# Optimization experiments

Measured on AMD Instinct MI355X. Metric: run time of the kernel, lower is better.

The kernel has to match this reference:

```python
import jax, jax.numpy as jnp
import numpy as np

B, CIN, HIN, WIN = 1, 26, 721, 1440
K, HOUT, KH, KW = 9, 360, 9, 9
COUT = 256
PSCALE = WIN // (WIN // 2)  # lon downsample stride = 2
WOUT = WIN // 2


def setup_inputs() -> dict:
    key = jax.random.key(0)
    k1, k2, k3 = jax.random.split(key, 3)
    x = jax.random.normal(k1, (B, CIN, HIN, WIN), dtype=jnp.float32)
    # precomputed basis*quadrature stencil psi[k, ho, dh, dw] (shift-invariant in lon,
    # stored only for wo=0, exactly as DISCO does). Normalized per (k, ho) ('mean' mode).
    psi = jax.random.normal(k2, (K, HOUT, KH, KW), dtype=jnp.float32)
    psi = psi / (jnp.mean(jnp.abs(psi), axis=(2, 3), keepdims=True) * (KH * KW) + 1e-6)
    weight = jax.random.normal(k3, (COUT, CIN, K), dtype=jnp.float32) * (1.0 / np.sqrt(CIN * K))
    # base input-lat row for each output lat (stencil top row), clipped to valid range
    hi_base = np.clip(np.round(np.arange(HOUT) * (HIN - 1) / HOUT).astype(np.int32) - KH // 2, 0, HIN - 1)
    return {"x": x, "psi": psi, "weight": weight, "hi_base": jnp.asarray(hi_base, dtype=jnp.int32)}


def _disco_conv(x, psi, weight, hi_base):
    x = x.astype(jnp.float32)  # fp32 autocast-off region, matches torch module
    acc = jnp.zeros((B, CIN, K, HOUT, WOUT), dtype=jnp.float32)
    for dh in range(KH):  # small structural loop over stencil rows
        rows = jnp.clip(hi_base + dh, 0, HIN - 1)  # [Hout]
        xr = x[:, :, rows, :]
        for dw in range(KW):  # small structural loop over stencil lon offsets
            shift = dw - KW // 2
            xs = jnp.roll(xr, -shift, axis=-1)[..., ::PSCALE]  # [B,C,Hout,Wout]
            acc = acc + psi[:, :, dh, dw][None, None, :, :, None] * xs[:, :, None, :, :]
    # contract learned weights over kernel basis and input channels
    out = jnp.einsum('bckhw,ock->bohw', acc, weight)  # [B,Cout,Hout,Wout]
    return out


def reference(x, psi, weight, hi_base):
    return _disco_conv(x, psi, weight, hi_base)
```

## Files before the change

kernel.cpp:

```cpp
#include <hip/hip_runtime.h>
#include <hip/hip_bf16.h>

#define CIN_   26
#define HIN_   721
#define WIN_   1440
#define K_     9
#define HOUT_  360
#define KH_    9
#define KW_    9
#define COUT_  256
#define WOUT_  720

#define WT     16
#define XSP    48
#define CCH    7
#define CK     (CIN_ * K_)
#define NKS2   9
#define ACCP2  296
#define NMT    (COUT_ / 16)
#define NXCD   8
#define HBAND  (HOUT_ / NXCD)

typedef short bf16x8 __attribute__((ext_vector_type(8)));
typedef float f32x4  __attribute__((ext_vector_type(4)));

__device__ unsigned short g_whi[NMT * NKS2 * 64 * 8];
__device__ unsigned short g_pfrag[HOUT_ * 3 * 64 * 8];

__device__ __forceinline__ unsigned short f2bf_rne(float f) {
    union { float f; unsigned u; } v; v.f = f;
    unsigned u = v.u;
    unsigned r = (u + 0x7FFFu + ((u >> 16) & 1u)) >> 16;
    return (unsigned short)r;
}
__device__ __forceinline__ unsigned pack_bf2(float a, float b) {
    const __hip_bfloat162 bv = __float22bfloat162_rn(make_float2(a, b));
    return *reinterpret_cast<const unsigned*>(&bv);
}

__global__ void prep_weight_kernel(const float* __restrict__ weight) {
    const int bid  = blockIdx.x;
    const int mt   = bid / NKS2;
    const int ks   = bid % NKS2;
    const int lane = threadIdx.x;
    const int row  = mt * 16 + (lane & 15);
    const int k0   = ks * 32 + (lane >> 4) * 8;
    const int base = ((mt * NKS2 + ks) * 64 + lane) * 8;
    #pragma unroll
    for (int j = 0; j < 8; ++j) {
        const int kp = k0 + j;
        float w = 0.f;
        if (kp < 260) {
            const int c = kp / 10, m = kp % 10;
            if (m < 9) w = weight[row * CK + c * 9 + m];
        }
        g_whi[base + j] = f2bf_rne(w);
    }
}

__global__ void prep_psi_kernel(const float* __restrict__ psi) {
    const int h    = blockIdx.x;
    const int lane = threadIdx.x;
    const int m    = lane & 15;
    const int kg   = lane >> 4;
    #pragma unroll
    for (int ks = 0; ks < 3; ++ks) {
        const int base = ((h * 3 + ks) * 64 + lane) * 8;
        #pragma unroll
        for (int e = 0; e < 8; ++e) {
            const int s = ks * 32 + kg * 8 + e;
            float v = 0.f;
            if (m < 9) {
                if (s < 72)      v = psi[(m * HOUT_ + h) * 81 + (s >> 3) * 9 + (s & 7)];
                else if (s < 81) v = psi[(m * HOUT_ + h) * 81 + (s - 72) * 9 + 8];
            }
            g_pfrag[base + e] = f2bf_rne(v);
        }
    }
}

__global__ __launch_bounds__(256, 8)
void disco_fused_kernel(const float* __restrict__ x,
                        const int*   __restrict__ hi_base,
                        float* __restrict__ out)
{
    __shared__ unsigned short xs_bf[CCH * KH_][XSP];
    __shared__ __align__(16) unsigned short acc_s[WT][ACCP2];

    const int b    = blockIdx.x;
    const int xcd  = b & (NXCD - 1);
    const int jb   = b >> 3;
    const int h    = xcd * HBAND + jb / 45;
    const int tile = jb % 45;
    const int w0   = tile * WT;
    const int tid  = threadIdx.x;

    const int hib = hi_base[h];

    #pragma unroll
    for (int t = 0; t < 2; ++t) {
        const int e = tid + t * 256;
        if (e < 16 * 28) acc_s[e / 28][260 + e % 28] = 0;
    }

    const int lane = tid & 63;
    const int wid  = tid >> 6;
    const int n    = lane & 15;
    const int kg   = lane >> 4;

    bf16x8 afrag[3];
    #pragma unroll
    for (int ks = 0; ks < 3; ++ks)
        afrag[ks] = *(const bf16x8*)&g_pfrag[((h * 3 + ks) * 64 + lane) * 8];

    const int c0 = 2 * w0 - 4;
    const char* xsb = (const char*)&xs_bf[0][0];

    for (int rd = 0; rd < 4; ++rd) {
        const int cbase = rd * CCH;
        const int nc    = (rd == 3) ? (CIN_ - 3 * CCH) : CCH;

        for (int i = tid; i < nc * KH_ * 10; i += 256) {
            const int q   = i % 10;
            const int lr  = i / 10;
            const int dh  = lr % KH_;
            const int c   = cbase + lr / KH_;
            int r = hib + dh;
            if (r > HIN_ - 1) r = HIN_ - 1;
            int g = c0 + 4 * q;
            if (g < 0)          g += WIN_;
            else if (g >= WIN_) g -= WIN_;
            const float4 v = *reinterpret_cast<const float4*>(x + ((size_t)c * HIN_ + r) * WIN_ + g);
            uint2 dv;
            dv.x = pack_bf2(v.x, v.y);
            dv.y = pack_bf2(v.z, v.w);
            *reinterpret_cast<uint2*>(&xs_bf[lr][4 * q]) = dv;
        }
        __syncthreads();

        for (int cc = wid; cc < nc; cc += 4) {
            const int c    = cbase + cc;
            const int base = cc * (KH_ * XSP * 2) + 4 * n;
            f32x4 C = {0.f, 0.f, 0.f, 0.f};
            #pragma unroll
            for (int ks = 0; ks < 3; ++ks) {
                union { bf16x8 v; unsigned d[4]; unsigned short u[8]; } bf;
                if (ks < 2 || kg == 0) {
                    const char* p = xsb + base + (ks * 4 + kg) * (XSP * 2);
                    #pragma unroll
                    for (int t = 0; t < 4; ++t)
                        bf.d[t] = *(const unsigned*)(p + 4 * t);
                } else if (kg == 1) {
                    #pragma unroll
                    for (int e = 0; e < 8; ++e)
                        bf.u[e] = *(const unsigned short*)(xsb + base + e * (XSP * 2) + 16);
                } else if (kg == 2) {
                    bf.d[0] = bf.d[1] = bf.d[2] = bf.d[3] = 0;
                    bf.u[0] = *(const unsigned short*)(xsb + base + 8 * (XSP * 2) + 16);
                } else {
                    bf.d[0] = bf.d[1] = bf.d[2] = bf.d[3] = 0;
                }
                C = __builtin_amdgcn_mfma_f32_16x16x32_bf16(afrag[ks], bf.v, C, 0, 0, 0);
            }
            if (kg < 2) {
                unsigned* ap = reinterpret_cast<unsigned*>(&acc_s[n][c * 10 + kg * 4]);
                ap[0] = pack_bf2(C[0], C[1]);
                ap[1] = pack_bf2(C[2], C[3]);
            } else if (kg == 2) {
                *reinterpret_cast<unsigned*>(&acc_s[n][c * 10 + 8]) = pack_bf2(C[0], 0.f);
            }
        }
        __syncthreads();
    }

    f32x4 C0 = {0.f, 0.f, 0.f, 0.f};
    f32x4 C1 = C0, C2 = C0, C3 = C0;

    const unsigned short* wp = g_whi + ((size_t)(wid * 4) * NKS2 * 64 + lane) * 8;

    bf16x8 wc[4];
    #pragma unroll
    for (int i = 0; i < 4; ++i)
        wc[i] = *(const bf16x8*)(wp + (size_t)i * NKS2 * 512);

    #pragma unroll
    for (int ks = 0; ks < NKS2; ++ks) {
        bf16x8 wn[4];
        if (ks + 1 < NKS2) {
            #pragma unroll
            for (int i = 0; i < 4; ++i)
                wn[i] = *(const bf16x8*)(wp + ((size_t)i * NKS2 + (ks + 1)) * 512);
        }
        const bf16x8 bhi = *(const bf16x8*)&acc_s[n][ks * 32 + kg * 8];
        C0 = __builtin_amdgcn_mfma_f32_16x16x32_bf16(wc[0], bhi, C0, 0, 0, 0);
        C1 = __builtin_amdgcn_mfma_f32_16x16x32_bf16(wc[1], bhi, C1, 0, 0, 0);
        C2 = __builtin_amdgcn_mfma_f32_16x16x32_bf16(wc[2], bhi, C2, 0, 0, 0);
        C3 = __builtin_amdgcn_mfma_f32_16x16x32_bf16(wc[3], bhi, C3, 0, 0, 0);
        if (ks + 1 < NKS2) {
            #pragma unroll
            for (int i = 0; i < 4; ++i) wc[i] = wn[i];
        }
    }

    #pragma unroll
    for (int i = 0; i < 4; ++i) {
        const f32x4 acc = (i == 0) ? C0 : (i == 1) ? C1 : (i == 2) ? C2 : C3;
        const int m0 = (wid * 4 + i) * 16 + kg * 4;
        #pragma unroll
        for (int r = 0; r < 4; ++r) {
            out[(size_t)(m0 + r) * (HOUT_ * WOUT_) + h * WOUT_ + w0 + n] = acc[r];
        }
    }
}

extern "C" void kernel_launch(void* const* d_in, const int* in_sizes, int n_in,
                              void* d_out, int out_size, void* d_ws, size_t ws_size,
                              hipStream_t stream)
{
    const float* x       = (const float*)d_in[0];
    const float* psi     = (const float*)d_in[1];
    const float* weight  = (const float*)d_in[2];
    const int*   hi_base = (const int*)d_in[3];
    float* out = (float*)d_out;

    hipLaunchKernelGGL(prep_weight_kernel, dim3(NMT * NKS2), dim3(64), 0, stream, weight);
    hipLaunchKernelGGL(prep_psi_kernel,    dim3(HOUT_),      dim3(64), 0, stream, psi);

    dim3 grid(45 * HOUT_, 1, 1);
    dim3 block(256, 1, 1);
    hipLaunchKernelGGL(disco_fused_kernel, grid, block, 0, stream,
                       x, hi_base, out);
}
```

Before: 257.3 us.

## Process three adjacent longitude tiles per block to reuse weight fragments

Each block now covers three consecutive 16-wide output longitude tiles instead of one, staging a wider bf16 input slab and keeping three per-tile bf16 accumulator buffers in shared memory. In the channel-mixing stage each weight fragment loaded from global memory feeds twelve MFMAs instead of four, which amortises the weight reads and the per-block setup (psi fragments, hi_base lookup). The grid shrinks to a third and the launch bound drops to 3 blocks per CU. Register and LDS use grow, so fewer waves can hide latency.

```diff
diff --git a/kernel.cpp b/kernel.cpp
--- a/kernel.cpp
+++ b/kernel.cpp
@@ -12,14 +12,15 @@
 #define WOUT_  720
 
 #define WT     16
-#define XSP    48
+#define TILES  3
+#define XCOLS3 104
+#define XSP3   104
 #define CCH    7
 #define CK     (CIN_ * K_)
 #define NKS2   9
 #define ACCP2  296
 #define NMT    (COUT_ / 16)
 #define NXCD   8
-#define HBAND  (HOUT_ / NXCD)
 
 typedef short bf16x8 __attribute__((ext_vector_type(8)));
 typedef float f32x4  __attribute__((ext_vector_type(4)));
@@ -79,28 +80,27 @@
     }
 }
 
-__global__ __launch_bounds__(256, 8)
+__global__ __launch_bounds__(256, 3)
 void disco_fused_kernel(const float* __restrict__ x,
                         const int*   __restrict__ hi_base,
                         float* __restrict__ out)
 {
-    __shared__ unsigned short xs_bf[CCH * KH_][XSP];
-    __shared__ __align__(16) unsigned short acc_s[WT][ACCP2];
-
-    const int b    = blockIdx.x;
-    const int xcd  = b & (NXCD - 1);
-    const int jb   = b >> 3;
-    const int h    = xcd * HBAND + jb / 45;
-    const int tile = jb % 45;
-    const int w0   = tile * WT;
-    const int tid  = threadIdx.x;
+    __shared__ unsigned short xs_bf[CCH * KH_][XSP3];
+    __shared__ __align__(16) unsigned short acc_s[TILES][WT][ACCP2];
+
+    const int b   = blockIdx.x;
+    const int xcd = b & (NXCD - 1);
+    const int j   = b >> 3;
+    const int h   = xcd * 45 + j / 15;
+    const int w0  = ((j % 15) * 3) * WT;
+    const int tid = threadIdx.x;
 
     const int hib = hi_base[h];
 
-    #pragma unroll
-    for (int t = 0; t < 2; ++t) {
-        const int e = tid + t * 256;
-        if (e < 16 * 28) acc_s[e / 28][260 + e % 28] = 0;
+    for (int e = tid; e < TILES * 16 * 14; e += 256) {
+        const int q  = e / 224;
+        const int r2 = e % 224;
+        *reinterpret_cast<unsigned*>(&acc_s[q][r2 / 14][260 + 2 * (r2 % 14)]) = 0u;
     }
 
     const int lane = tid & 63;
@@ -120,11 +120,11 @@
         const int cbase = rd * CCH;
         const int nc    = (rd == 3) ? (CIN_ - 3 * CCH) : CCH;
 
-        for (int i = tid; i < nc * KH_ * 10; i += 256) {
-            const int q   = i % 10;
-            const int lr  = i / 10;
-            const int dh  = lr % KH_;
-            const int c   = cbase + lr / KH_;
+        for (int i = tid; i < nc * KH_ * (XCOLS3 / 4); i += 256) {
+            const int q  = i % (XCOLS3 / 4);
+            const int lr = i / (XCOLS3 / 4);
+            const int dh = lr % KH_;
+            const int c  = cbase + lr / KH_;
             int r = hib + dh;
             if (r > HIN_ - 1) r = HIN_ - 1;
             int g = c0 + 4 * q;
@@ -140,41 +140,66 @@
 
         for (int cc = wid; cc < nc; cc += 4) {
             const int c    = cbase + cc;
-            const int base = cc * (KH_ * XSP * 2) + 4 * n;
-            f32x4 C = {0.f, 0.f, 0.f, 0.f};
+            const int rowb = cc * (KH_ * XSP3 * 2);
+            f32x4 ct0 = {0.f, 0.f, 0.f, 0.f}, ct1 = ct0, ct2 = ct0;
+
             #pragma unroll
             for (int ks = 0; ks < 3; ++ks) {
-                union { bf16x8 v; unsigned d[4]; unsigned short u[8]; } bf;
-                if (ks < 2 || kg == 0) {
-                    const char* p = xsb + base + (ks * 4 + kg) * (XSP * 2);
-                    #pragma unroll
-                    for (int t = 0; t < 4; ++t)
-                        bf.d[t] = *(const unsigned*)(p + 4 * t);
-                } else if (kg == 1) {
-                    #pragma unroll
-                    for (int e = 0; e < 8; ++e)
-                        bf.u[e] = *(const unsigned short*)(xsb + base + e * (XSP * 2) + 16);
-                } else if (kg == 2) {
-                    bf.d[0] = bf.d[1] = bf.d[2] = bf.d[3] = 0;
-                    bf.u[0] = *(const unsigned short*)(xsb + base + 8 * (XSP * 2) + 16);
-                } else {
-                    bf.d[0] = bf.d[1] = bf.d[2] = bf.d[3] = 0;
-                }
-                C = __builtin_amdgcn_mfma_f32_16x16x32_bf16(afrag[ks], bf.v, C, 0, 0, 0);
+                #define P1_TILE(CQ, QQ)                                                          \
+                do {                                                                             \
+                    union { bf16x8 v; unsigned d[4]; unsigned short u[8]; } bf;                  \
+                    const int tb = rowb + 64 * (QQ) + 4 * n;                                     \
+                    if (ks < 2 || kg == 0) {                                                     \
+                        const char* p = xsb + tb + (ks * 4 + kg) * (XSP3 * 2);                   \
+                        bf.d[0] = *(const unsigned*)(p);                                         \
+                        bf.d[1] = *(const unsigned*)(p + 4);                                     \
+                        bf.d[2] = *(const unsigned*)(p + 8);                                     \
+                        bf.d[3] = *(const unsigned*)(p + 12);                                    \
+                    } else if (kg == 1) {                                                        \
+                        _Pragma("unroll")                                                        \
+                        for (int e = 0; e < 8; ++e)                                              \
+                            bf.u[e] = *(const unsigned short*)(xsb + tb + e * (XSP3 * 2) + 16);  \
+                    } else if (kg == 2) {                                                        \
+                        bf.d[0] = bf.d[1] = bf.d[2] = bf.d[3] = 0;                               \
+                        bf.u[0] = *(const unsigned short*)(xsb + tb + 8 * (XSP3 * 2) + 16);      \
+                    } else {                                                                     \
+                        bf.d[0] = bf.d[1] = bf.d[2] = bf.d[3] = 0;                               \
+                    }                                                                            \
+                    CQ = __builtin_amdgcn_mfma_f32_16x16x32_bf16(afrag[ks], bf.v, CQ, 0, 0, 0);  \
+                } while (0)
+
+                P1_TILE(ct0, 0);
+                P1_TILE(ct1, 1);
+                P1_TILE(ct2, 2);
+                #undef P1_TILE
             }
-            if (kg < 2) {
-                unsigned* ap = reinterpret_cast<unsigned*>(&acc_s[n][c * 10 + kg * 4]);
-                ap[0] = pack_bf2(C[0], C[1]);
-                ap[1] = pack_bf2(C[2], C[3]);
-            } else if (kg == 2) {
-                *reinterpret_cast<unsigned*>(&acc_s[n][c * 10 + 8]) = pack_bf2(C[0], 0.f);
-            }
+
+            #define P1_WB(CQ, QQ)                                                                \
+            do {                                                                                 \
+                if (kg < 2) {                                                                    \
+                    unsigned* ap = reinterpret_cast<unsigned*>(&acc_s[QQ][n][c * 10 + kg * 4]);  \
+                    ap[0] = pack_bf2(CQ[0], CQ[1]);                                              \
+                    ap[1] = pack_bf2(CQ[2], CQ[3]);                                              \
+                } else if (kg == 2) {                                                            \
+                    *reinterpret_cast<unsigned*>(&acc_s[QQ][n][c * 10 + 8]) =                    \
+                        pack_bf2(CQ[0], 0.f);                                                    \
+                }                                                                                \
+            } while (0)
+
+            P1_WB(ct0, 0);
+            P1_WB(ct1, 1);
+            P1_WB(ct2, 2);
+            #undef P1_WB
         }
         __syncthreads();
     }
 
-    f32x4 C0 = {0.f, 0.f, 0.f, 0.f};
-    f32x4 C1 = C0, C2 = C0, C3 = C0;
+    f32x4 C[TILES][4];
+    #pragma unroll
+    for (int q = 0; q < TILES; ++q)
+        #pragma unroll
+        for (int i = 0; i < 4; ++i)
+            C[q][i] = (f32x4){0.f, 0.f, 0.f, 0.f};
 
     const unsigned short* wp = g_whi + ((size_t)(wid * 4) * NKS2 * 64 + lane) * 8;
 
@@ -191,11 +216,14 @@
             for (int i = 0; i < 4; ++i)
                 wn[i] = *(const bf16x8*)(wp + ((size_t)i * NKS2 + (ks + 1)) * 512);
         }
-        const bf16x8 bhi = *(const bf16x8*)&acc_s[n][ks * 32 + kg * 8];
-        C0 = __builtin_amdgcn_mfma_f32_16x16x32_bf16(wc[0], bhi, C0, 0, 0, 0);
-        C1 = __builtin_amdgcn_mfma_f32_16x16x32_bf16(wc[1], bhi, C1, 0, 0, 0);
-        C2 = __builtin_amdgcn_mfma_f32_16x16x32_bf16(wc[2], bhi, C2, 0, 0, 0);
-        C3 = __builtin_amdgcn_mfma_f32_16x16x32_bf16(wc[3], bhi, C3, 0, 0, 0);
+        #pragma unroll
+        for (int q = 0; q < TILES; ++q) {
+            const bf16x8 bq = *(const bf16x8*)&acc_s[q][n][ks * 32 + kg * 8];
+            C[q][0] = __builtin_amdgcn_mfma_f32_16x16x32_bf16(wc[0], bq, C[q][0], 0, 0, 0);
+            C[q][1] = __builtin_amdgcn_mfma_f32_16x16x32_bf16(wc[1], bq, C[q][1], 0, 0, 0);
+            C[q][2] = __builtin_amdgcn_mfma_f32_16x16x32_bf16(wc[2], bq, C[q][2], 0, 0, 0);
+            C[q][3] = __builtin_amdgcn_mfma_f32_16x16x32_bf16(wc[3], bq, C[q][3], 0, 0, 0);
+        }
         if (ks + 1 < NKS2) {
             #pragma unroll
             for (int i = 0; i < 4; ++i) wc[i] = wn[i];
@@ -203,12 +231,14 @@
     }
 
     #pragma unroll
-    for (int i = 0; i < 4; ++i) {
-        const f32x4 acc = (i == 0) ? C0 : (i == 1) ? C1 : (i == 2) ? C2 : C3;
-        const int m0 = (wid * 4 + i) * 16 + kg * 4;
-        #pragma unroll
-        for (int r = 0; r < 4; ++r) {
-            out[(size_t)(m0 + r) * (HOUT_ * WOUT_) + h * WOUT_ + w0 + n] = acc[r];
+    for (int q = 0; q < TILES; ++q) {
+        #pragma unroll
+        for (int i = 0; i < 4; ++i) {
+            const int m0 = (wid * 4 + i) * 16 + kg * 4;
+            #pragma unroll
+            for (int r = 0; r < 4; ++r) {
+                out[(size_t)(m0 + r) * (HOUT_ * WOUT_) + h * WOUT_ + w0 + q * WT + n] = C[q][i][r];
+            }
         }
     }
 }
@@ -226,7 +256,7 @@
     hipLaunchKernelGGL(prep_weight_kernel, dim3(NMT * NKS2), dim3(64), 0, stream, weight);
     hipLaunchKernelGGL(prep_psi_kernel,    dim3(HOUT_),      dim3(64), 0, stream, psi);
 
-    dim3 grid(45 * HOUT_, 1, 1);
+    dim3 grid(5400, 1, 1);
     dim3 block(256, 1, 1);
     hipLaunchKernelGGL(disco_fused_kernel, grid, block, 0, stream,
                        x, hi_base, out);
```

Measured after the change: 263.1 us. +2.3%, slower.

## Double-buffer input tile in LDS with register prefetch across channel rounds

Applied to the files above, without the earlier changes.

Replaces the per-round load-then-sync loop with a software pipeline. Global float4 loads for the next channel round are issued into registers before the current round's MFMA work, then written to an alternate LDS buffer. Barriers become a lighter custom waitcnt-plus-s_barrier. This is meant to hide global load latency behind the stencil MFMA work, at the cost of double the xs_bf LDS footprint, more live registers, and a lower launch-bounds occupancy target (8 to 6).

```diff
diff --git a/kernel.cpp b/kernel.cpp
--- a/kernel.cpp
+++ b/kernel.cpp
@@ -79,12 +79,18 @@
     }
 }
 
-__global__ __launch_bounds__(256, 8)
+#define LDS_BARRIER()                                      \
+    do {                                                   \
+        asm volatile("s_waitcnt lgkmcnt(0)" ::: "memory"); \
+        __builtin_amdgcn_s_barrier();                      \
+    } while (0)
+
+__global__ __launch_bounds__(256, 6)
 void disco_fused_kernel(const float* __restrict__ x,
                         const int*   __restrict__ hi_base,
                         float* __restrict__ out)
 {
-    __shared__ unsigned short xs_bf[CCH * KH_][XSP];
+    __shared__ unsigned short xs_bf[2][CCH * KH_][XSP];
     __shared__ __align__(16) unsigned short acc_s[WT][ACCP2];
 
     const int b    = blockIdx.x;
@@ -114,32 +120,58 @@
         afrag[ks] = *(const bf16x8*)&g_pfrag[((h * 3 + ks) * 64 + lane) * 8];
 
     const int c0 = 2 * w0 - 4;
-    const char* xsb = (const char*)&xs_bf[0][0];
-
+
+    #define ISSUE(RD, V, S)                                                          \
+    do {                                                                             \
+        const int items = ((RD) == 3) ? 450 : 630;                                   \
+        _Pragma("unroll")                                                            \
+        for (int t = 0; t < 3; ++t) {                                                \
+            const int i  = tid + t * 256;                                            \
+            const int ii = (i < items) ? i : (items - 1);                            \
+            const int q  = ii % 10;                                                  \
+            const int lr = ii / 10;                                                  \
+            const int dh = lr % 9;                                                   \
+            const int c  = (RD) * CCH + lr / 9;                                      \
+            int r = hib + dh;                                                        \
+            if (r > HIN_ - 1) r = HIN_ - 1;                                          \
+            int g = c0 + 4 * q;                                                      \
+            if (g < 0)          g += WIN_;                                           \
+            else if (g >= WIN_) g -= WIN_;                                           \
+            V[t] = *reinterpret_cast<const float4*>(                                 \
+                x + ((size_t)c * HIN_ + r) * WIN_ + g);                              \
+            S[t] = (i < items) ? (lr * XSP + 4 * q) : -1;                            \
+        }                                                                            \
+    } while (0)
+
+    #define WRITE(RD, V, S)                                                          \
+    do {                                                                             \
+        unsigned short* dst = &xs_bf[(RD) & 1][0][0];                                \
+        _Pragma("unroll")                                                            \
+        for (int t = 0; t < 3; ++t) {                                                \
+            if (S[t] >= 0) {                                                         \
+                uint2 dv;                                                            \
+                dv.x = pack_bf2(V[t].x, V[t].y);                                     \
+                dv.y = pack_bf2(V[t].z, V[t].w);                                     \
+                *reinterpret_cast<uint2*>(dst + S[t]) = dv;                          \
+            }                                                                        \
+        }                                                                            \
+    } while (0)
+
+    float4 va[3], vb[3];
+    int    sa[3], sb[3];
+
+    ISSUE(0, va, sa);
+    WRITE(0, va, sa);
+    ISSUE(1, vb, sb);
+    LDS_BARRIER();
+
+    #pragma unroll
     for (int rd = 0; rd < 4; ++rd) {
-        const int cbase = rd * CCH;
-        const int nc    = (rd == 3) ? (CIN_ - 3 * CCH) : CCH;
-
-        for (int i = tid; i < nc * KH_ * 10; i += 256) {
-            const int q   = i % 10;
-            const int lr  = i / 10;
-            const int dh  = lr % KH_;
-            const int c   = cbase + lr / KH_;
-            int r = hib + dh;
-            if (r > HIN_ - 1) r = HIN_ - 1;
-            int g = c0 + 4 * q;
-            if (g < 0)          g += WIN_;
-            else if (g >= WIN_) g -= WIN_;
-            const float4 v = *reinterpret_cast<const float4*>(x + ((size_t)c * HIN_ + r) * WIN_ + g);
-            uint2 dv;
-            dv.x = pack_bf2(v.x, v.y);
-            dv.y = pack_bf2(v.z, v.w);
-            *reinterpret_cast<uint2*>(&xs_bf[lr][4 * q]) = dv;
-        }
-        __syncthreads();
+        const int nc = (rd == 3) ? (CIN_ - 3 * CCH) : CCH;
+        const char* xsb = (const char*)&xs_bf[rd & 1][0][0];
 
         for (int cc = wid; cc < nc; cc += 4) {
-            const int c    = cbase + cc;
+            const int c    = rd * CCH + cc;
             const int base = cc * (KH_ * XSP * 2) + 4 * n;
             f32x4 C = {0.f, 0.f, 0.f, 0.f};
             #pragma unroll
@@ -170,8 +202,14 @@
                 *reinterpret_cast<unsigned*>(&acc_s[n][c * 10 + 8]) = pack_bf2(C[0], 0.f);
             }
         }
-        __syncthreads();
-    }
+
+        if (rd == 0)      { WRITE(1, vb, sb); ISSUE(2, va, sa); }
+        else if (rd == 1) { WRITE(2, va, sa); ISSUE(3, vb, sb); }
+        else if (rd == 2) { WRITE(3, vb, sb); }
+        LDS_BARRIER();
+    }
+    #undef ISSUE
+    #undef WRITE
 
     f32x4 C0 = {0.f, 0.f, 0.f, 0.f};
     f32x4 C1 = C0, C2 = C0, C3 = C0;
```

Measured after the change: 256.9 us. Within noise of the previous version (-0.1%).

## Double-buffer input tiles via async global-to-LDS loads, convert to bf16 on read

Applied to the files above, without the earlier changes.

Replaces the synchronous register-staged fp32→bf16 load of input rows into LDS with asynchronous global_load_lds DMA into two fp32 LDS buffers. The next channel group is prefetched while the current one is consumed. Conversion to bf16 now happens when fragments are read from LDS. This aims to hide global load latency behind the stencil MFMA work, at the cost of more LDS per block (launch bound occupancy lowered from 8 to 4) and extra conversions in the inner loop.

```diff
diff --git a/kernel.cpp b/kernel.cpp
--- a/kernel.cpp
+++ b/kernel.cpp
@@ -12,7 +12,7 @@
 #define WOUT_  720
 
 #define WT     16
-#define XSP    48
+#define XFP    40
 #define CCH    7
 #define CK     (CIN_ * K_)
 #define NKS2   9
@@ -36,6 +36,12 @@
 __device__ __forceinline__ unsigned pack_bf2(float a, float b) {
     const __hip_bfloat162 bv = __float22bfloat162_rn(make_float2(a, b));
     return *reinterpret_cast<const unsigned*>(&bv);
+}
+__device__ __forceinline__ void gload_lds16(const float* g, float* l) {
+    __builtin_amdgcn_global_load_lds(
+        (const __attribute__((address_space(1))) void*)g,
+        (__attribute__((address_space(3))) void*)l,
+        16, 0, 0);
 }
 
 __global__ void prep_weight_kernel(const float* __restrict__ weight) {
@@ -79,12 +85,19 @@
     }
 }
 
-__global__ __launch_bounds__(256, 8)
+#define LDS_BARRIER()                                      \
+    do {                                                   \
+        asm volatile("s_waitcnt lgkmcnt(0)" ::: "memory"); \
+        __builtin_amdgcn_s_barrier();                      \
+    } while (0)
+#define VM_WAIT(N) asm volatile("s_waitcnt vmcnt(" #N ")" ::: "memory")
+
+__global__ __launch_bounds__(256, 4)
 void disco_fused_kernel(const float* __restrict__ x,
                         const int*   __restrict__ hi_base,
                         float* __restrict__ out)
 {
-    __shared__ unsigned short xs_bf[CCH * KH_][XSP];
+    __shared__ float xs_f[2][12 * 256];
     __shared__ __align__(16) unsigned short acc_s[WT][ACCP2];
 
     const int b    = blockIdx.x;
@@ -112,51 +125,63 @@
     #pragma unroll
     for (int ks = 0; ks < 3; ++ks)
         afrag[ks] = *(const bf16x8*)&g_pfrag[((h * 3 + ks) * 64 + lane) * 8];
+    VM_WAIT(0);
 
     const int c0 = 2 * w0 - 4;
-    const char* xsb = (const char*)&xs_bf[0][0];
-
+
+    #define ISSUE_DMA(RD, BUF, RMAX)                                             \
+    do {                                                                         \
+        const int cb = (RD) * CCH;                                               \
+        _Pragma("unroll")                                                        \
+        for (int it = 0; it < 3; ++it) {                                         \
+            const int g64 = wid + 4 * it;                                        \
+            const int ii  = g64 * 64 + lane;                                     \
+            int row = ii / 10;                                                   \
+            const int q = ii - row * 10;                                         \
+            if (row > (RMAX)) row = (RMAX);                                      \
+            const int dh = row % 9;                                              \
+            const int c  = cb + row / 9;                                         \
+            int r = hib + dh;                                                    \
+            if (r > HIN_ - 1) r = HIN_ - 1;                                      \
+            int gc = c0 + 4 * q;                                                 \
+            if (gc < 0)          gc += WIN_;                                     \
+            else if (gc >= WIN_) gc -= WIN_;                                     \
+            gload_lds16(x + ((size_t)c * HIN_ + r) * WIN_ + gc,                  \
+                        &xs_f[BUF][g64 * 256]);                                  \
+        }                                                                        \
+    } while (0)
+
+    ISSUE_DMA(0, 0, 62);
+    ISSUE_DMA(1, 1, 62);
+    VM_WAIT(3);
+    LDS_BARRIER();
+
+    #pragma unroll
     for (int rd = 0; rd < 4; ++rd) {
-        const int cbase = rd * CCH;
-        const int nc    = (rd == 3) ? (CIN_ - 3 * CCH) : CCH;
-
-        for (int i = tid; i < nc * KH_ * 10; i += 256) {
-            const int q   = i % 10;
-            const int lr  = i / 10;
-            const int dh  = lr % KH_;
-            const int c   = cbase + lr / KH_;
-            int r = hib + dh;
-            if (r > HIN_ - 1) r = HIN_ - 1;
-            int g = c0 + 4 * q;
-            if (g < 0)          g += WIN_;
-            else if (g >= WIN_) g -= WIN_;
-            const float4 v = *reinterpret_cast<const float4*>(x + ((size_t)c * HIN_ + r) * WIN_ + g);
-            uint2 dv;
-            dv.x = pack_bf2(v.x, v.y);
-            dv.y = pack_bf2(v.z, v.w);
-            *reinterpret_cast<uint2*>(&xs_bf[lr][4 * q]) = dv;
-        }
-        __syncthreads();
+        const int nc = (rd == 3) ? (CIN_ - 3 * CCH) : CCH;
+        const float* xsf = &xs_f[rd & 1][0];
 
         for (int cc = wid; cc < nc; cc += 4) {
-            const int c    = cbase + cc;
-            const int base = cc * (KH_ * XSP * 2) + 4 * n;
+            const int c = rd * CCH + cc;
+            const float* rbase = xsf + (cc * 9) * XFP + 2 * n;
             f32x4 C = {0.f, 0.f, 0.f, 0.f};
             #pragma unroll
             for (int ks = 0; ks < 3; ++ks) {
                 union { bf16x8 v; unsigned d[4]; unsigned short u[8]; } bf;
                 if (ks < 2 || kg == 0) {
-                    const char* p = xsb + base + (ks * 4 + kg) * (XSP * 2);
+                    const float* rp = rbase + (ks * 4 + kg) * XFP;
                     #pragma unroll
-                    for (int t = 0; t < 4; ++t)
-                        bf.d[t] = *(const unsigned*)(p + 4 * t);
+                    for (int t = 0; t < 4; ++t) {
+                        const float2 v2 = *reinterpret_cast<const float2*>(rp + 2 * t);
+                        bf.d[t] = pack_bf2(v2.x, v2.y);
+                    }
                 } else if (kg == 1) {
                     #pragma unroll
                     for (int e = 0; e < 8; ++e)
-                        bf.u[e] = *(const unsigned short*)(xsb + base + e * (XSP * 2) + 16);
+                        bf.u[e] = f2bf_rne(rbase[e * XFP + 8]);
                 } else if (kg == 2) {
                     bf.d[0] = bf.d[1] = bf.d[2] = bf.d[3] = 0;
-                    bf.u[0] = *(const unsigned short*)(xsb + base + 8 * (XSP * 2) + 16);
+                    bf.u[0] = f2bf_rne(rbase[8 * XFP + 8]);
                 } else {
                     bf.d[0] = bf.d[1] = bf.d[2] = bf.d[3] = 0;
                 }
@@ -170,8 +195,25 @@
                 *reinterpret_cast<unsigned*>(&acc_s[n][c * 10 + 8]) = pack_bf2(C[0], 0.f);
             }
         }
-        __syncthreads();
-    }
+
+        if (rd == 0) {
+            LDS_BARRIER();
+            ISSUE_DMA(2, 0, 62);
+            VM_WAIT(3);
+            LDS_BARRIER();
+        } else if (rd == 1) {
+            LDS_BARRIER();
+            ISSUE_DMA(3, 1, 44);
+            VM_WAIT(3);
+            LDS_BARRIER();
+        } else if (rd == 2) {
+            LDS_BARRIER();
+            VM_WAIT(0);
+            LDS_BARRIER();
+        }
+    }
+    #undef ISSUE_DMA
+    LDS_BARRIER();
 
     f32x4 C0 = {0.f, 0.f, 0.f, 0.f};
     f32x4 C1 = C0, C2 = C0, C3 = C0;
```

Result: no change. 257.1 us (-0.1%).
